# Kernel optimization log

Hardware: AMD Instinct MI355X
Metric: run time of the kernel (lower is better)

The kernel has to match this reference:

```python
import jax, jax.numpy as jnp
from jax import lax
import numpy as np

N_BITS = 108
N_OUT = 7
# pos_bits[i, j] = bit j (MSB-first) of index i, matching `i >> (6 - j) & 1`
POS_BITS = np.array([[(i >> (6 - j)) & 1 for j in range(N_OUT)] for i in range(N_BITS)], dtype=np.float32)
# LZC value when all 108 bits are zero: 108 = 1101100b, MSB first
LZC_108 = np.array([1, 1, 0, 1, 1, 0, 0], dtype=np.float32)


def setup_inputs() -> dict:
    key = jax.random.key(0)
    # sparse binary bits so leading-zero runs are long and some rows are all-zero
    X = (jax.random.uniform(key, (2_000_000, N_BITS)) < 0.03).astype(jnp.float32)
    return {"X": X}


def _lzd(X):
    """X: [..., 108] MSB-first bits -> [..., 7] LZC MSB-first.

    Arithmetic soft-gate semantics: NOT(a)=1-a, AND(a,b)=a*b,
    OR(a,b)=a+b-a*b, MUX(s,a,b)=s*a+(1-s)*b, OR-tree = 1-prod(1-x).
    Sequential carry over `found` expressed with lax.scan (108 steps).
    """
    batch_shape = X.shape[:-1]
    bits = jnp.moveaxis(X, -1, 0)  # [108, ...]
    pos = jnp.asarray(POS_BITS, dtype=X.dtype)  # [108, 7]

    def step(carry, inp):
        found, lzc = carry                  # found: [..., 1], lzc: [..., 7]
        bit, pos_bits = inp                 # bit: [...], pos_bits: [7]
        bit = bit[..., None]                # [..., 1]
        not_found = 1.0 - found             # NOT
        is_first = bit * not_found          # AND
        # MUX per output bit: is_first ? pos_bit : lzc
        lzc = is_first * pos_bits + (1.0 - is_first) * lzc
        # OR: found | is_first
        found = found + is_first - found * is_first
        return (found, lzc), None

    found0 = jnp.zeros(batch_shape + (1,), X.dtype)
    lzc0 = jnp.zeros(batch_shape + (N_OUT,), X.dtype)
    (found, lzc), _ = lax.scan(step, (found0, lzc0), (bits, pos))

    # OR-tree over all 108 bits, then all-zero override with LZC=108
    any_one = 1.0 - jnp.prod(1.0 - X, axis=-1, keepdims=True)  # [..., 1]
    all_zero = 1.0 - any_one                                   # NOT
    lzc108 = jnp.asarray(LZC_108, dtype=X.dtype)               # [7]
    return all_zero * lzc108 + (1.0 - all_zero) * lzc


def reference(X):
    return _lzd(X)
```

## Files before the change

kernel.cpp:

```cpp
#include <hip/hip_runtime.h>


#define LZD_NBITS 108
#define LZD_NOUT 7

__global__ __launch_bounds__(256) void lzd108_kernel(const float* __restrict__ X,
                                                     float* __restrict__ out,
                                                     int n_rows) {
    int row = blockIdx.x * blockDim.x + threadIdx.x;
    if (row >= n_rows) return;

    const float4* p = reinterpret_cast<const float4*>(X + (size_t)row * LZD_NBITS);

    int idx = -1;

    #pragma unroll 1
    for (int c = 0; c < 6; ++c) {
        float4 v0 = p[4 * c + 0];
        float4 v1 = p[4 * c + 1];
        float4 v2 = p[4 * c + 2];
        float4 v3 = p[4 * c + 3];
        unsigned m = 0u;
        m |= (v0.x != 0.0f) ? (1u << 0)  : 0u;
        m |= (v0.y != 0.0f) ? (1u << 1)  : 0u;
        m |= (v0.z != 0.0f) ? (1u << 2)  : 0u;
        m |= (v0.w != 0.0f) ? (1u << 3)  : 0u;
        m |= (v1.x != 0.0f) ? (1u << 4)  : 0u;
        m |= (v1.y != 0.0f) ? (1u << 5)  : 0u;
        m |= (v1.z != 0.0f) ? (1u << 6)  : 0u;
        m |= (v1.w != 0.0f) ? (1u << 7)  : 0u;
        m |= (v2.x != 0.0f) ? (1u << 8)  : 0u;
        m |= (v2.y != 0.0f) ? (1u << 9)  : 0u;
        m |= (v2.z != 0.0f) ? (1u << 10) : 0u;
        m |= (v2.w != 0.0f) ? (1u << 11) : 0u;
        m |= (v3.x != 0.0f) ? (1u << 12) : 0u;
        m |= (v3.y != 0.0f) ? (1u << 13) : 0u;
        m |= (v3.z != 0.0f) ? (1u << 14) : 0u;
        m |= (v3.w != 0.0f) ? (1u << 15) : 0u;
        if (m) {
            idx = 16 * c + (__ffs(m) - 1);
            break;
        }
    }

    if (idx < 0) {
        float4 v0 = p[24];
        float4 v1 = p[25];
        float4 v2 = p[26];
        unsigned m = 0u;
        m |= (v0.x != 0.0f) ? (1u << 0)  : 0u;
        m |= (v0.y != 0.0f) ? (1u << 1)  : 0u;
        m |= (v0.z != 0.0f) ? (1u << 2)  : 0u;
        m |= (v0.w != 0.0f) ? (1u << 3)  : 0u;
        m |= (v1.x != 0.0f) ? (1u << 4)  : 0u;
        m |= (v1.y != 0.0f) ? (1u << 5)  : 0u;
        m |= (v1.z != 0.0f) ? (1u << 6)  : 0u;
        m |= (v1.w != 0.0f) ? (1u << 7)  : 0u;
        m |= (v2.x != 0.0f) ? (1u << 8)  : 0u;
        m |= (v2.y != 0.0f) ? (1u << 9)  : 0u;
        m |= (v2.z != 0.0f) ? (1u << 10) : 0u;
        m |= (v2.w != 0.0f) ? (1u << 11) : 0u;
        idx = m ? (96 + (__ffs(m) - 1)) : LZD_NBITS;
    }

    float* o = out + (size_t)row * LZD_NOUT;
    o[0] = (float)((idx >> 6) & 1);
    o[1] = (float)((idx >> 5) & 1);
    o[2] = (float)((idx >> 4) & 1);
    o[3] = (float)((idx >> 3) & 1);
    o[4] = (float)((idx >> 2) & 1);
    o[5] = (float)((idx >> 1) & 1);
    o[6] = (float)(idx & 1);
}

extern "C" void kernel_launch(void* const* d_in, const int* in_sizes, int n_in,
                              void* d_out, int out_size, void* d_ws, size_t ws_size,
                              hipStream_t stream) {
    const float* X = (const float*)d_in[0];
    float* out = (float*)d_out;
    int n_rows = in_sizes[0] / LZD_NBITS;
    int block = 256;
    int grid = (n_rows + block - 1) / block;
    lzd108_kernel<<<grid, block, 0, stream>>>(X, out, n_rows);
}
```

Before: 1.026 ms.

## Coalesce row loads across block into shared bitmasks and stage output writes

Instead of each thread walking its own 432-byte row with strided float4 loads and early exit, the block cooperatively loads its 256 rows with fully coalesced float4 accesses and ORs nonzero flags into per-row shared-memory bitmasks. Each thread then finds the first set bit of its row and writes its 7 outputs into a shared buffer, which is copied out with coalesced float4 stores. This gives up the early-exit read savings and adds LDS atomics and barriers in exchange for contiguous global memory traffic.

```diff
diff --git a/kernel.cpp b/kernel.cpp
--- a/kernel.cpp
+++ b/kernel.cpp
@@ -1,85 +1,110 @@
 #include <hip/hip_runtime.h>
 
 
-#define LZD_NBITS 108
-#define LZD_NOUT 7
+#define NBITS 108
+#define NOUT 7
+#define RPB 256
+#define F4_PER_ROW 27
+#define F4_PER_BLOCK (RPB * F4_PER_ROW)
 
-__global__ __launch_bounds__(256) void lzd108_kernel(const float* __restrict__ X,
+__global__ __launch_bounds__(256) void lzd108_kernel(const float4* __restrict__ X4,
                                                      float* __restrict__ out,
                                                      int n_rows) {
-    int row = blockIdx.x * blockDim.x + threadIdx.x;
-    if (row >= n_rows) return;
+    __shared__ unsigned masks[RPB][4];
+    __shared__ __align__(16) float obuf[RPB * NOUT];
 
-    const float4* p = reinterpret_cast<const float4*>(X + (size_t)row * LZD_NBITS);
+    const int tid = threadIdx.x;
+    const long long block_row0 = (long long)blockIdx.x * RPB;
 
-    int idx = -1;
+    masks[tid][0] = 0u;
+    masks[tid][1] = 0u;
+    masks[tid][2] = 0u;
+    masks[tid][3] = 0u;
+    __syncthreads();
 
-    #pragma unroll 1
-    for (int c = 0; c < 6; ++c) {
-        float4 v0 = p[4 * c + 0];
-        float4 v1 = p[4 * c + 1];
-        float4 v2 = p[4 * c + 2];
-        float4 v3 = p[4 * c + 3];
-        unsigned m = 0u;
-        m |= (v0.x != 0.0f) ? (1u << 0)  : 0u;
-        m |= (v0.y != 0.0f) ? (1u << 1)  : 0u;
-        m |= (v0.z != 0.0f) ? (1u << 2)  : 0u;
-        m |= (v0.w != 0.0f) ? (1u << 3)  : 0u;
-        m |= (v1.x != 0.0f) ? (1u << 4)  : 0u;
-        m |= (v1.y != 0.0f) ? (1u << 5)  : 0u;
-        m |= (v1.z != 0.0f) ? (1u << 6)  : 0u;
-        m |= (v1.w != 0.0f) ? (1u << 7)  : 0u;
-        m |= (v2.x != 0.0f) ? (1u << 8)  : 0u;
-        m |= (v2.y != 0.0f) ? (1u << 9)  : 0u;
-        m |= (v2.z != 0.0f) ? (1u << 10) : 0u;
-        m |= (v2.w != 0.0f) ? (1u << 11) : 0u;
-        m |= (v3.x != 0.0f) ? (1u << 12) : 0u;
-        m |= (v3.y != 0.0f) ? (1u << 13) : 0u;
-        m |= (v3.z != 0.0f) ? (1u << 14) : 0u;
-        m |= (v3.w != 0.0f) ? (1u << 15) : 0u;
-        if (m) {
-            idx = 16 * c + (__ffs(m) - 1);
-            break;
+    int rows_here = n_rows - (int)block_row0;
+    if (rows_here > RPB) rows_here = RPB;
+    const bool full = (rows_here == RPB);
+
+    const float4* base = X4 + block_row0 * F4_PER_ROW;
+    const int total_f4 = rows_here * F4_PER_ROW;
+
+    if (full) {
+        #pragma unroll
+        for (int i = 0; i < F4_PER_ROW; ++i) {
+            const int q = i * RPB + tid;
+            float4 v = base[q];
+            unsigned m = 0u;
+            m |= (v.x != 0.0f) ? 1u : 0u;
+            m |= (v.y != 0.0f) ? 2u : 0u;
+            m |= (v.z != 0.0f) ? 4u : 0u;
+            m |= (v.w != 0.0f) ? 8u : 0u;
+            if (m) {
+                const int local_row = q / F4_PER_ROW;
+                const int bit0 = (q - local_row * F4_PER_ROW) * 4;
+                atomicOr(&masks[local_row][bit0 >> 5], m << (bit0 & 31));
+            }
+        }
+    } else {
+        for (int q = tid; q < total_f4; q += RPB) {
+            float4 v = base[q];
+            unsigned m = 0u;
+            m |= (v.x != 0.0f) ? 1u : 0u;
+            m |= (v.y != 0.0f) ? 2u : 0u;
+            m |= (v.z != 0.0f) ? 4u : 0u;
+            m |= (v.w != 0.0f) ? 8u : 0u;
+            if (m) {
+                const int local_row = q / F4_PER_ROW;
+                const int bit0 = (q - local_row * F4_PER_ROW) * 4;
+                atomicOr(&masks[local_row][bit0 >> 5], m << (bit0 & 31));
+            }
         }
     }
+    __syncthreads();
 
-    if (idx < 0) {
-        float4 v0 = p[24];
-        float4 v1 = p[25];
-        float4 v2 = p[26];
-        unsigned m = 0u;
-        m |= (v0.x != 0.0f) ? (1u << 0)  : 0u;
-        m |= (v0.y != 0.0f) ? (1u << 1)  : 0u;
-        m |= (v0.z != 0.0f) ? (1u << 2)  : 0u;
-        m |= (v0.w != 0.0f) ? (1u << 3)  : 0u;
-        m |= (v1.x != 0.0f) ? (1u << 4)  : 0u;
-        m |= (v1.y != 0.0f) ? (1u << 5)  : 0u;
-        m |= (v1.z != 0.0f) ? (1u << 6)  : 0u;
-        m |= (v1.w != 0.0f) ? (1u << 7)  : 0u;
-        m |= (v2.x != 0.0f) ? (1u << 8)  : 0u;
-        m |= (v2.y != 0.0f) ? (1u << 9)  : 0u;
-        m |= (v2.z != 0.0f) ? (1u << 10) : 0u;
-        m |= (v2.w != 0.0f) ? (1u << 11) : 0u;
-        idx = m ? (96 + (__ffs(m) - 1)) : LZD_NBITS;
+    if (tid < rows_here) {
+        const unsigned w0 = masks[tid][0];
+        const unsigned w1 = masks[tid][1];
+        const unsigned w2 = masks[tid][2];
+        const unsigned w3 = masks[tid][3];
+        int idx;
+        if (w0)      idx =       __ffs(w0) - 1;
+        else if (w1) idx = 32  + __ffs(w1) - 1;
+        else if (w2) idx = 64  + __ffs(w2) - 1;
+        else if (w3) idx = 96  + __ffs(w3) - 1;
+        else         idx = NBITS;
+        float* o = &obuf[tid * NOUT];
+        o[0] = (float)((idx >> 6) & 1);
+        o[1] = (float)((idx >> 5) & 1);
+        o[2] = (float)((idx >> 4) & 1);
+        o[3] = (float)((idx >> 3) & 1);
+        o[4] = (float)((idx >> 2) & 1);
+        o[5] = (float)((idx >> 1) & 1);
+        o[6] = (float)(idx & 1);
     }
+    __syncthreads();
 
-    float* o = out + (size_t)row * LZD_NOUT;
-    o[0] = (float)((idx >> 6) & 1);
-    o[1] = (float)((idx >> 5) & 1);
-    o[2] = (float)((idx >> 4) & 1);
-    o[3] = (float)((idx >> 3) & 1);
-    o[4] = (float)((idx >> 2) & 1);
-    o[5] = (float)((idx >> 1) & 1);
-    o[6] = (float)(idx & 1);
+    float* gout = out + block_row0 * NOUT;
+    if (full) {
+        float4* g4 = reinterpret_cast<float4*>(gout);
+        const float4* s4 = reinterpret_cast<const float4*>(obuf);
+        #pragma unroll
+        for (int i = 0; i < (RPB * NOUT) / 4 / RPB + 1; ++i) {
+            const int q = i * RPB + tid;
+            if (q < (RPB * NOUT) / 4) g4[q] = s4[q];
+        }
+    } else {
+        const int total_f = rows_here * NOUT;
+        for (int q = tid; q < total_f; q += RPB) gout[q] = obuf[q];
+    }
 }
 
 extern "C" void kernel_launch(void* const* d_in, const int* in_sizes, int n_in,
                               void* d_out, int out_size, void* d_ws, size_t ws_size,
                               hipStream_t stream) {
-    const float* X = (const float*)d_in[0];
+    const float4* X4 = (const float4*)d_in[0];
     float* out = (float*)d_out;
-    int n_rows = in_sizes[0] / LZD_NBITS;
-    int block = 256;
-    int grid = (n_rows + block - 1) / block;
-    lzd108_kernel<<<grid, block, 0, stream>>>(X, out, n_rows);
+    const int n_rows = in_sizes[0] / NBITS;
+    const int grid = (n_rows + RPB - 1) / RPB;
+    lzd108_kernel<<<grid, RPB, 0, stream>>>(X4, out, n_rows);
 }
```

New measurement: 1.084 ms. 1.06x slower.

## Assign four rows per wavefront with coalesced loads and ballot-based first-bit search

Applied to the files above, without the earlier changes.

Each row was handled by one thread reading with large strides and exiting early. The kernel now gives a group of four rows to each wavefront: lanes load consecutive uint4 words, so reads are coalesced. Ballot and readlane then find the first nonzero word per row, and the outputs are written coalesced by lane. It also switches to a fixed 4096-block grid-stride launch. The trade-off is that every row is read in full, dropping the early exit, and the integer nonzero test would count -0.0 as set.

```diff
diff --git a/kernel.cpp b/kernel.cpp
--- a/kernel.cpp
+++ b/kernel.cpp
@@ -1,85 +1,75 @@
 #include <hip/hip_runtime.h>
 
 
-#define LZD_NBITS 108
-#define LZD_NOUT 7
+#define NBITS 108
+#define NOUT 7
+#define F4R 27
 
-__global__ __launch_bounds__(256) void lzd108_kernel(const float* __restrict__ X,
+__global__ __launch_bounds__(256) void lzd108_kernel(const uint4* __restrict__ X4,
                                                      float* __restrict__ out,
                                                      int n_rows) {
-    int row = blockIdx.x * blockDim.x + threadIdx.x;
-    if (row >= n_rows) return;
+    const int lane = threadIdx.x & 63;
+    const long long wave    = (long long)blockIdx.x * 4 + (threadIdx.x >> 6);
+    const long long nwaves  = (long long)gridDim.x * 4;
+    const long long ngroups = ((long long)n_rows + 3) >> 2;
 
-    const float4* p = reinterpret_cast<const float4*>(X + (size_t)row * LZD_NBITS);
+    for (long long g = wave; g < ngroups; g += nwaves) {
+        const long long row0 = g << 2;
+        int rows_here = (int)(n_rows - row0);
+        if (rows_here > 4) rows_here = 4;
+        const int act0 = (rows_here >= 2 ? 2 : rows_here) * F4R;
+        const int act1 = (rows_here > 2 ? rows_here - 2 : 0) * F4R;
 
-    int idx = -1;
+        const uint4* base = X4 + row0 * F4R;
+        unsigned m0 = 0u, m1 = 0u;
+        if (lane < act0) {
+            uint4 v = base[lane];
+            m0 = (v.x ? 1u : 0u) | (v.y ? 2u : 0u) | (v.z ? 4u : 0u) | (v.w ? 8u : 0u);
+        }
+        if (lane < act1) {
+            uint4 v = base[54 + lane];
+            m1 = (v.x ? 1u : 0u) | (v.y ? 2u : 0u) | (v.z ? 4u : 0u) | (v.w ? 8u : 0u);
+        }
+        const unsigned long long nz0 = __ballot(m0 != 0u);
+        const unsigned long long nz1 = __ballot(m1 != 0u);
 
-    #pragma unroll 1
-    for (int c = 0; c < 6; ++c) {
-        float4 v0 = p[4 * c + 0];
-        float4 v1 = p[4 * c + 1];
-        float4 v2 = p[4 * c + 2];
-        float4 v3 = p[4 * c + 3];
-        unsigned m = 0u;
-        m |= (v0.x != 0.0f) ? (1u << 0)  : 0u;
-        m |= (v0.y != 0.0f) ? (1u << 1)  : 0u;
-        m |= (v0.z != 0.0f) ? (1u << 2)  : 0u;
-        m |= (v0.w != 0.0f) ? (1u << 3)  : 0u;
-        m |= (v1.x != 0.0f) ? (1u << 4)  : 0u;
-        m |= (v1.y != 0.0f) ? (1u << 5)  : 0u;
-        m |= (v1.z != 0.0f) ? (1u << 6)  : 0u;
-        m |= (v1.w != 0.0f) ? (1u << 7)  : 0u;
-        m |= (v2.x != 0.0f) ? (1u << 8)  : 0u;
-        m |= (v2.y != 0.0f) ? (1u << 9)  : 0u;
-        m |= (v2.z != 0.0f) ? (1u << 10) : 0u;
-        m |= (v2.w != 0.0f) ? (1u << 11) : 0u;
-        m |= (v3.x != 0.0f) ? (1u << 12) : 0u;
-        m |= (v3.y != 0.0f) ? (1u << 13) : 0u;
-        m |= (v3.z != 0.0f) ? (1u << 14) : 0u;
-        m |= (v3.w != 0.0f) ? (1u << 15) : 0u;
-        if (m) {
-            idx = 16 * c + (__ffs(m) - 1);
-            break;
+        int i0 = NBITS, i1 = NBITS, i2 = NBITS, i3 = NBITS;
+        {
+            const unsigned long long a = nz0 & 0x7FFFFFFull;
+            if (a) { const int l = __ffsll(a) - 1;
+                     const unsigned mm = __builtin_amdgcn_readlane(m0, l);
+                     i0 = l * 4 + __ffs(mm) - 1; }
+            const unsigned long long b = (nz0 >> 27) & 0x7FFFFFFull;
+            if (b) { const int l = __ffsll(b) - 1;
+                     const unsigned mm = __builtin_amdgcn_readlane(m0, l + 27);
+                     i1 = l * 4 + __ffs(mm) - 1; }
+            const unsigned long long c = nz1 & 0x7FFFFFFull;
+            if (c) { const int l = __ffsll(c) - 1;
+                     const unsigned mm = __builtin_amdgcn_readlane(m1, l);
+                     i2 = l * 4 + __ffs(mm) - 1; }
+            const unsigned long long d = (nz1 >> 27) & 0x7FFFFFFull;
+            if (d) { const int l = __ffsll(d) - 1;
+                     const unsigned mm = __builtin_amdgcn_readlane(m1, l + 27);
+                     i3 = l * 4 + __ffs(mm) - 1; }
+        }
+
+        if (lane < NOUT * rows_here) {
+            const int r = lane / NOUT;
+            const int j = lane - r * NOUT;
+            const int id01 = (r == 0) ? i0 : i1;
+            const int id23 = (r == 2) ? i2 : i3;
+            const int id = (r < 2) ? id01 : id23;
+            out[row0 * NOUT + lane] = (float)((id >> (6 - j)) & 1);
         }
     }
-
-    if (idx < 0) {
-        float4 v0 = p[24];
-        float4 v1 = p[25];
-        float4 v2 = p[26];
-        unsigned m = 0u;
-        m |= (v0.x != 0.0f) ? (1u << 0)  : 0u;
-        m |= (v0.y != 0.0f) ? (1u << 1)  : 0u;
-        m |= (v0.z != 0.0f) ? (1u << 2)  : 0u;
-        m |= (v0.w != 0.0f) ? (1u << 3)  : 0u;
-        m |= (v1.x != 0.0f) ? (1u << 4)  : 0u;
-        m |= (v1.y != 0.0f) ? (1u << 5)  : 0u;
-        m |= (v1.z != 0.0f) ? (1u << 6)  : 0u;
-        m |= (v1.w != 0.0f) ? (1u << 7)  : 0u;
-        m |= (v2.x != 0.0f) ? (1u << 8)  : 0u;
-        m |= (v2.y != 0.0f) ? (1u << 9)  : 0u;
-        m |= (v2.z != 0.0f) ? (1u << 10) : 0u;
-        m |= (v2.w != 0.0f) ? (1u << 11) : 0u;
-        idx = m ? (96 + (__ffs(m) - 1)) : LZD_NBITS;
-    }
-
-    float* o = out + (size_t)row * LZD_NOUT;
-    o[0] = (float)((idx >> 6) & 1);
-    o[1] = (float)((idx >> 5) & 1);
-    o[2] = (float)((idx >> 4) & 1);
-    o[3] = (float)((idx >> 3) & 1);
-    o[4] = (float)((idx >> 2) & 1);
-    o[5] = (float)((idx >> 1) & 1);
-    o[6] = (float)(idx & 1);
 }
 
 extern "C" void kernel_launch(void* const* d_in, const int* in_sizes, int n_in,
                               void* d_out, int out_size, void* d_ws, size_t ws_size,
                               hipStream_t stream) {
-    const float* X = (const float*)d_in[0];
+    const uint4* X4 = (const uint4*)d_in[0];
     float* out = (float*)d_out;
-    int n_rows = in_sizes[0] / LZD_NBITS;
-    int block = 256;
-    int grid = (n_rows + block - 1) / block;
-    lzd108_kernel<<<grid, block, 0, stream>>>(X, out, n_rows);
+    const int n_rows = in_sizes[0] / NBITS;
+    const int grid = 4096;
+    lzd108_kernel<<<grid, 256, 0, stream>>>(X4, out, n_rows);
 }
```

Result: slower. 1.095 ms (+6.8%).
